# Kernel optimization log

Hardware: AMD Instinct MI355X
Metric: run time of the kernel (lower is better)

The kernel has to match this reference:

```python
import jax, jax.numpy as jnp
import numpy as np

N, C, H, W = 4, 128, 64, 64
HEADS, KS, RED = 4, 7, 18
D = C // HEADS


def _layernorm(x, w, b, eps=1e-5):
    mu = x.mean(axis=-1, keepdims=True)
    var = ((x - mu) ** 2).mean(axis=-1, keepdims=True)
    return (x - mu) * jax.lax.rsqrt(var + eps) * w + b


def _gelu(x):
    return jax.nn.gelu(x, approximate=False)


def setup_inputs() -> dict:
    key = jax.random.key(0)
    ks = jax.random.split(key, 16)
    s = 0.02
    inp = {
        'x': jax.random.normal(ks[0], (N, C, H, W), jnp.float32),
        'ln1_w': jnp.ones((C,), jnp.float32), 'ln1_b': jnp.zeros((C,), jnp.float32),
        'ln2_w': jnp.ones((C,), jnp.float32), 'ln2_b': jnp.zeros((C,), jnp.float32),
        'qkv_w': jax.random.normal(ks[1], (C, 3 * C), jnp.float32) * s,
        'qkv_b': jnp.zeros((3 * C,), jnp.float32),
        'proj_w': jax.random.normal(ks[2], (C, C), jnp.float32) * s,
        'proj_b': jnp.zeros((C,), jnp.float32),
        'rpb': jax.random.normal(ks[3], (HEADS, 2 * KS - 1, 2 * KS - 1), jnp.float32) * s,
        'conv1_w': jax.random.normal(ks[4], (C, C // 4), jnp.float32) * s,
        'conv1_b': jnp.zeros((C // 4,), jnp.float32),
        'conv2_w': jax.random.normal(ks[5], (C // 4, C), jnp.float32) * s,
        'conv2_b': jnp.zeros((C,), jnp.float32),
        'ca1_w': jax.random.normal(ks[6], (C, C // RED), jnp.float32) * s,
        'ca1_b': jnp.zeros((C // RED,), jnp.float32),
        'ca2_w': jax.random.normal(ks[7], (C // RED, C), jnp.float32) * s,
        'ca2_b': jnp.zeros((C,), jnp.float32),
        'fc1_w': jax.random.normal(ks[8], (C, 4 * C), jnp.float32) * s,
        'fc1_b': jnp.zeros((4 * C,), jnp.float32),
        'fc2_w': jax.random.normal(ks[9], (4 * C, C), jnp.float32) * s,
        'fc2_b': jnp.zeros((C,), jnp.float32),
    }
    return inp


def _na2d(xc, qkv_w, qkv_b, rpb, proj_w, proj_b):
    # xc: [N, H, W, C] -> neighborhood attention with clamped k x k windows (NATTEN semantics)
    n, h, w, c = xc.shape
    qkv = (xc @ qkv_w + qkv_b).reshape(n, h, w, 3, HEADS, D)
    q, k, v = qkv[..., 0, :, :], qkv[..., 1, :, :], qkv[..., 2, :, :]
    q = q * (D ** -0.5)
    half = KS // 2
    ni = jnp.clip(jnp.arange(h) - half, 0, h - KS)          # window start per query row
    nj = jnp.clip(jnp.arange(w) - half, 0, w - KS)
    idx_i = ni[:, None] + jnp.arange(KS)                     # [H, KS]
    idx_j = nj[:, None] + jnp.arange(KS)                     # [W, KS]
    # gather key/value windows: [N, H, KS, W, KS, heads, D]
    kw = k[:, idx_i][:, :, :, idx_j]
    vw = v[:, idx_i][:, :, :, idx_j]
    attn = jnp.einsum('nijhd,niajbhd->nijhab', q, kw)        # [N,H,W,heads,KS,KS]
    bi = idx_i - jnp.arange(h)[:, None] + (KS - 1)           # rel-pos bias row index [H,KS]
    bj = idx_j - jnp.arange(w)[:, None] + (KS - 1)           # [W,KS]
    bias = rpb[:, bi][:, :, :, bj]                           # [heads,H,KS,W,KS]
    attn = attn + bias.transpose(1, 3, 0, 2, 4)[None]        # -> [1,H,W,heads,KS,KS]
    attn = jax.nn.softmax(attn.reshape(n, h, w, HEADS, KS * KS), axis=-1)
    attn = attn.reshape(n, h, w, HEADS, KS, KS)
    out = jnp.einsum('nijhab,niajbhd->nijhd', attn, vw).reshape(n, h, w, c)
    return out @ proj_w + proj_b


def reference(x, ln1_w, ln1_b, ln2_w, ln2_b, qkv_w, qkv_b, proj_w, proj_b, rpb,
              conv1_w, conv1_b, conv2_w, conv2_b, ca1_w, ca1_b, ca2_w, ca2_b,
              fc1_w, fc1_b, fc2_w, fc2_b):
    n, c, h, w = x.shape
    xs = x.transpose(0, 2, 3, 1).reshape(n, h * w, c)        # n (h w) c
    shortcut = xs
    xn = _layernorm(xs, ln1_w, ln1_b)
    xc = xn.reshape(n, h, w, c)
    # conv branch: 1x1 -> GELU -> 1x1 -> channel attention
    t = _gelu(xc @ conv1_w + conv1_b) @ conv2_w + conv2_b
    g = t.mean(axis=(1, 2))                                  # global avg pool [N,C]
    g = jax.nn.sigmoid(jax.nn.relu(g @ ca1_w + ca1_b) @ ca2_w + ca2_b)
    ca_x = (t * g[:, None, None, :]).reshape(n, h * w, c)
    # neighborhood attention branch
    na_x = _na2d(xc, qkv_w, qkv_b, rpb, proj_w, proj_b).reshape(n, h * w, c)
    x2 = shortcut + na_x + ca_x * 0.02
    m = _gelu(_layernorm(x2, ln2_w, ln2_b) @ fc1_w + fc1_b) @ fc2_w + fc2_b
    x3 = x2 + m
    return x3.reshape(n, h, w, c).transpose(0, 3, 1, 2)
```

## Files before the change

kernel.cpp:

```cpp
#include <hip/hip_runtime.h>
#include <hip/hip_bf16.h>
#include <math.h>

#define NB 4
#define CC 128
#define HH 64
#define WW 64
#define HEADS 4
#define KS 7
#define DD 32
#define HW 4096
#define MTOT 16384

typedef unsigned short BF;
typedef short short8 __attribute__((ext_vector_type(8)));
typedef float floatx4 __attribute__((ext_vector_type(4)));

__device__ __forceinline__ float gelu_f(float x) {
    return 0.5f * x * (1.0f + erff(x * 0.70710678118654752440f));
}

__device__ __forceinline__ BF f2bf(float f) {
    union { float f; unsigned u; } a; a.f = f;
    unsigned u = a.u;
    unsigned r = u + 0x7FFFu + ((u >> 16) & 1u);
    return (BF)(r >> 16);
}

__device__ __forceinline__ float bf2f(BF v) {
    return __uint_as_float(((unsigned)v) << 16);
}

#define LDK 40
#define LDK128 136

__global__ __launch_bounds__(256) void ln1t_kernel(
    const float* __restrict__ x, const float* __restrict__ w,
    const float* __restrict__ b, BF* __restrict__ out,
    float* __restrict__ part,
    const float* __restrict__ qkv_w, const float* __restrict__ conv1_w,
    const float* __restrict__ conv2_w, const float* __restrict__ proj_w,
    const float* __restrict__ fc1_w, const float* __restrict__ fc2_w,
    BF* __restrict__ qkvT, BF* __restrict__ c1T, BF* __restrict__ c2T,
    BF* __restrict__ projT, BF* __restrict__ fc1T, BF* __restrict__ fc2T)
{
    const int blk = blockIdx.x;
    const int t  = threadIdx.x;

    if (blk >= 512) {
        for (int idx = (blk - 512) * 256 + t; idx < 204800; idx += 32768) {
            if (idx < 49152) {
                int l = idx, n = l >> 7, k = l & 127;
                qkvT[l] = f2bf(qkv_w[k * 384 + n]);
            } else if (idx < 53248) {
                int l = idx - 49152, n = l >> 7, k = l & 127;
                c1T[l] = f2bf(conv1_w[k * 32 + n]);
            } else if (idx < 57344) {
                int l = idx - 53248, n = l >> 5, k = l & 31;
                c2T[l] = f2bf(conv2_w[k * 128 + n]);
            } else if (idx < 73728) {
                int l = idx - 57344, n = l >> 7, k = l & 127;
                projT[l] = f2bf(proj_w[k * 128 + n]);
            } else if (idx < 139264) {
                int l = idx - 73728, n = l >> 7, k = l & 127;
                fc1T[l] = f2bf(fc1_w[k * 512 + n]);
            } else {
                int l = idx - 139264, n = l >> 9, k = l & 511;
                fc2T[l] = f2bf(fc2_w[k * 128 + n]);
            }
        }
        return;
    }

    __shared__ float xt[128][33];
    __shared__ float mus[32], rss[32];
    const int n  = blk >> 7;
    const int p0 = (blk & 127) * 32;
    if (blk < 4 && t < 128) part[blk * CC + t] = 0.f;

    {
        int pp = t & 31, c8 = t >> 5;
        #pragma unroll 4
        for (int it = 0; it < 16; it++) {
            int c = it * 8 + c8;
            xt[c][pp] = x[(size_t)(n * CC + c) * HW + p0 + pp];
        }
    }
    __syncthreads();
    {
        int pp2 = t >> 3, cb = t & 7;
        float s = 0.f;
        #pragma unroll
        for (int u = 0; u < 16; u++) s += xt[cb + u * 8][pp2];
        s += __shfl_xor(s, 1); s += __shfl_xor(s, 2); s += __shfl_xor(s, 4);
        float mu = s * (1.0f / CC);
        float v = 0.f;
        #pragma unroll
        for (int u = 0; u < 16; u++) { float d = xt[cb + u * 8][pp2] - mu; v += d * d; }
        v += __shfl_xor(v, 1); v += __shfl_xor(v, 2); v += __shfl_xor(v, 4);
        if (cb == 0) { mus[pp2] = mu; rss[pp2] = rsqrtf(v * (1.0f / CC) + 1e-5f); }
    }
    __syncthreads();
    {
        #pragma unroll
        for (int it = 0; it < 2; it++) {
            int pp2 = (t >> 4) + it * 16;
            int c0  = (t & 15) * 8;
            float mu = mus[pp2], rs = rss[pp2];
            int m = n * HW + p0 + pp2;
            short8 o;
            #pragma unroll
            for (int u = 0; u < 8; u++)
                o[u] = (short)f2bf((xt[c0 + u][pp2] - mu) * rs * w[c0 + u] + b[c0 + u]);
            *(short8*)(out + (size_t)m * CC + c0) = o;
        }
    }
}

template<int ACT>
__device__ __forceinline__ void k128_body(
    const BF* __restrict__ A, const BF* __restrict__ Bt,
    const float* __restrict__ bias, BF* __restrict__ Cout,
    int N, int row0, int col0, BF* Bl )
{
    const int t = threadIdx.x;
    const int w = t >> 6, lane = t & 63, q = lane >> 4, r16 = lane & 15;
    {
        int nn = t >> 2;
        int kk = (t & 3) * 32;
        const BF* src = Bt + (size_t)(col0 + nn) * 128 + kk;
        #pragma unroll
        for (int u = 0; u < 4; u++)
            *(uint4*)(Bl + nn * LDK128 + kk + u * 8) = *(const uint4*)(src + u * 8);
    }
    __syncthreads();
    floatx4 acc[4] = {};
    const BF* arow = A + (size_t)(row0 + w * 16 + r16) * CC;
    #pragma unroll
    for (int ks = 0; ks < 4; ks++) {
        short8 af = *(const short8*)(arow + ks * 32 + q * 8);
        #pragma unroll
        for (int nt = 0; nt < 4; nt++) {
            short8 bf = *(const short8*)(Bl + (nt * 16 + r16) * LDK128 + ks * 32 + q * 8);
            acc[nt] = __builtin_amdgcn_mfma_f32_16x16x32_bf16(af, bf, acc[nt], 0, 0, 0);
        }
    }
    #pragma unroll
    for (int nt = 0; nt < 4; nt++) {
        int col = col0 + nt * 16 + r16;
        float bv = bias[col];
        #pragma unroll
        for (int reg = 0; reg < 4; reg++) {
            int row = row0 + w * 16 + q * 4 + reg;
            float v = acc[nt][reg] + bv;
            if (ACT == 1) v = gelu_f(v);
            Cout[(size_t)row * N + col] = f2bf(v);
        }
    }
}

__global__ __launch_bounds__(256) void phase2(
    const BF* __restrict__ xn, const BF* __restrict__ qkvT,
    const float* __restrict__ qkv_b, BF* __restrict__ qkv_out,
    const BF* __restrict__ c1T, const float* __restrict__ b1,
    const BF* __restrict__ c2T, const float* __restrict__ b2,
    BF* __restrict__ tout, float* __restrict__ part)
{
    __shared__ __align__(16) char smem[26624];
    const int bid = blockIdx.x;
    const int t = threadIdx.x;
    const int w = t >> 6, lane = t & 63, q = lane >> 4, r16 = lane & 15;

    if (bid < 1536) {
        int col0 = (bid % 6) * 64;
        int row0 = (bid / 6) * 64;
        k128_body<0>(xn, qkvT, qkv_b, qkv_out, 384, row0, col0, (BF*)smem);
        return;
    }
    BF*    W1l = (BF*)smem;
    BF*    W2l = (BF*)(smem + 8704);
    BF*    Hl  = (BF*)(smem + 18944);
    float* red = (float*)(smem + 24064);
    const int row0 = (bid - 1536) * 64;
    {
        #pragma unroll
        for (int it = 0; it < 2; it++) {
            int idx = it * 256 + t;
            int nn = idx >> 4, u = idx & 15;
            *(uint4*)(W1l + nn * LDK128 + u * 8) = *(const uint4*)(c1T + nn * 128 + u * 8);
        }
    }
    {
        #pragma unroll
        for (int it = 0; it < 2; it++) {
            int idx = it * 256 + t;
            int nn = idx >> 2, u = idx & 3;
            *(uint4*)(W2l + nn * LDK + u * 8) = *(const uint4*)(c2T + nn * 32 + u * 8);
        }
    }
    __syncthreads();
    floatx4 a1[2] = {};
    const BF* arow = xn + (size_t)(row0 + w * 16 + r16) * CC;
    #pragma unroll
    for (int ks = 0; ks < 4; ks++) {
        short8 af = *(const short8*)(arow + ks * 32 + q * 8);
        #pragma unroll
        for (int nt = 0; nt < 2; nt++) {
            short8 bf = *(const short8*)(W1l + (nt * 16 + r16) * LDK128 + ks * 32 + q * 8);
            a1[nt] = __builtin_amdgcn_mfma_f32_16x16x32_bf16(af, bf, a1[nt], 0, 0, 0);
        }
    }
    #pragma unroll
    for (int nt = 0; nt < 2; nt++) {
        int col = nt * 16 + r16;
        float bv = b1[col];
        #pragma unroll
        for (int reg = 0; reg < 4; reg++)
            Hl[(w * 16 + q * 4 + reg) * LDK + col] = f2bf(gelu_f(a1[nt][reg] + bv));
    }
    __syncthreads();
    floatx4 a2[8] = {};
    short8 af2 = *(const short8*)(Hl + (w * 16 + r16) * LDK + q * 8);
    #pragma unroll
    for (int nt = 0; nt < 8; nt++) {
        short8 bf = *(const short8*)(W2l + (nt * 16 + r16) * LDK + q * 8);
        a2[nt] = __builtin_amdgcn_mfma_f32_16x16x32_bf16(af2, bf, a2[nt], 0, 0, 0);
    }
    #pragma unroll
    for (int nt = 0; nt < 8; nt++) {
        int col = nt * 16 + r16;
        float bv = b2[col];
        float s = 0.f;
        #pragma unroll
        for (int reg = 0; reg < 4; reg++) {
            int row = row0 + w * 16 + q * 4 + reg;
            float v = a2[nt][reg] + bv;
            tout[(size_t)row * CC + col] = f2bf(v);
            s += v;
        }
        s += __shfl_xor(s, 16);
        s += __shfl_xor(s, 32);
        if (lane < 16) red[w * 128 + col] = s;
    }
    __syncthreads();
    if (t < 128) {
        float cs = red[t] + red[128 + t] + red[256 + t] + red[384 + t];
        atomicAdd(&part[(row0 >> 12) * CC + t], cs);
    }
}

template<int ACT>
__global__ __launch_bounds__(256) void gemm_k128(
    const BF* __restrict__ A, const BF* __restrict__ Bt,
    const float* __restrict__ bias, BF* __restrict__ Cout, int N)
{
    __shared__ __align__(16) BF Bl[64 * LDK128];
    k128_body<ACT>(A, Bt, bias, Cout, N, blockIdx.y * 64, blockIdx.x * 64, Bl);
}

__global__ __launch_bounds__(256) void na_mfma_kernel(
    const BF* __restrict__ qkv, const float* __restrict__ rpb,
    BF* __restrict__ outp)
{
    __shared__ __align__(16) BF Kt[224][40];
    __shared__ __align__(16) BF Vt[32][232];
    __shared__ __align__(16) BF Qb[64][40];
    __shared__ __align__(16) BF Pl[4][16][232];
    __shared__ float rb[169];

    const int b = blockIdx.x;
    const int h = b & 3;
    const int tile = b >> 2;
    const int n = tile >> 6;
    const int ti = (tile >> 3) & 7, tj = tile & 7;
    const int t = threadIdx.x;
    const int w = t >> 6, lane = t & 63, quad = lane >> 4, r16 = lane & 15;
    const int i0 = ti * 8, j0 = tj * 8;
    const int wi0 = max(i0 - 3, 0), wj0 = max(j0 - 3, 0);
    const int R  = min(wi0 + 13, 63) - wi0 + 1;
    const int Rj = min(wj0 + 13, 63) - wj0 + 1;

    for (int idx = t; idx < 896; idx += 256) {
        int key = idx >> 2, ch = idx & 3;
        int kr = key >> 4, kc = key & 15;
        uint4 v = {0u, 0u, 0u, 0u};
        if (kr < R && kc < Rj) {
            size_t pix = (size_t)((n * HH + wi0 + kr) * WW + wj0 + kc);
            v = *(const uint4*)(qkv + pix * 384 + 128 + h * DD + ch * 8);
        }
        *(uint4*)&Kt[key][ch * 8] = v;
    }
    for (int idx = t; idx < 896; idx += 256) {
        int key = idx >> 2, ch = idx & 3;
        int kr = key >> 4, kc = key & 15;
        if (kr < R && kc < Rj) {
            size_t pix = (size_t)((n * HH + wi0 + kr) * WW + wj0 + kc);
            uint4 v = *(const uint4*)(qkv + pix * 384 + 256 + h * DD + ch * 8);
            const BF* pv = (const BF*)&v;
            #pragma unroll
            for (int u = 0; u < 8; u++) Vt[ch * 8 + u][key] = pv[u];
        } else {
            #pragma unroll
            for (int u = 0; u < 8; u++) Vt[ch * 8 + u][key] = 0;
        }
    }
    {
        int q = t >> 2, ch = t & 3;
        size_t mq = (size_t)((n * HH + i0 + (q >> 3)) * WW + j0 + (q & 7));
        *(uint4*)&Qb[q][ch * 8] = *(const uint4*)(qkv + mq * 384 + h * DD + ch * 8);
    }
    if (t < 169) rb[t] = rpb[h * 169 + t];
    __syncthreads();

    int oi[4], cok[4], bj0[4], ai_[4];
    #pragma unroll
    for (int reg = 0; reg < 4; reg++) {
        int q = w * 16 + quad * 4 + reg;
        int i = i0 + (q >> 3), j = j0 + (q & 7);
        int ni = min(max(i - 3, 0), HH - KS), nj = min(max(j - 3, 0), WW - KS);
        oi[reg]  = ni - wi0;
        ai_[reg] = ni - i + 6;
        int dc = r16 - (nj - wj0);
        cok[reg] = ((unsigned)dc < 7u) ? 1 : 0;
        bj0[reg] = min(max(dc + (nj - j + 6), 0), 12);
    }

    short8 aq = *(const short8*)&Qb[w * 16 + r16][quad * 8];
    floatx4 S[14];
    #pragma unroll
    for (int nt = 0; nt < 14; nt++) {
        floatx4 z = {0.f, 0.f, 0.f, 0.f};
        short8 bk = *(const short8*)&Kt[nt * 16 + r16][quad * 8];
        S[nt] = __builtin_amdgcn_mfma_f32_16x16x32_bf16(aq, bk, z, 0, 0, 0);
    }
    const float scale = 0.17677669529663688110f;
    #pragma unroll
    for (int nt = 0; nt < 14; nt++) {
        #pragma unroll
        for (int reg = 0; reg < 4; reg++) {
            int dr = nt - oi[reg];
            bool ok = ((unsigned)dr < 7u) && cok[reg];
            int bi = min(max(dr + ai_[reg], 0), 12);
            float bias = rb[bi * 13 + bj0[reg]];
            S[nt][reg] = ok ? fmaf(S[nt][reg], scale, bias) : -1e30f;
        }
    }
    float rinv[4];
    #pragma unroll
    for (int reg = 0; reg < 4; reg++) {
        float m = S[0][reg];
        #pragma unroll
        for (int nt = 1; nt < 14; nt++) m = fmaxf(m, S[nt][reg]);
        m = fmaxf(m, __shfl_xor(m, 1));
        m = fmaxf(m, __shfl_xor(m, 2));
        m = fmaxf(m, __shfl_xor(m, 4));
        m = fmaxf(m, __shfl_xor(m, 8));
        float s = 0.f;
        #pragma unroll
        for (int nt = 0; nt < 14; nt++) {
            float e = __expf(S[nt][reg] - m);
            S[nt][reg] = e;
            s += e;
        }
        s += __shfl_xor(s, 1);
        s += __shfl_xor(s, 2);
        s += __shfl_xor(s, 4);
        s += __shfl_xor(s, 8);
        rinv[reg] = 1.0f / s;
    }
    #pragma unroll
    for (int nt = 0; nt < 14; nt++)
        #pragma unroll
        for (int reg = 0; reg < 4; reg++)
            Pl[w][quad * 4 + reg][nt * 16 + r16] = f2bf(S[nt][reg] * rinv[reg]);

    floatx4 O0 = {0.f, 0.f, 0.f, 0.f}, O1 = {0.f, 0.f, 0.f, 0.f};
    #pragma unroll
    for (int ks = 0; ks < 7; ks++) {
        short8 ap = *(const short8*)&Pl[w][r16][ks * 32 + quad * 8];
        short8 b0 = *(const short8*)&Vt[r16][ks * 32 + quad * 8];
        short8 b1 = *(const short8*)&Vt[16 + r16][ks * 32 + quad * 8];
        O0 = __builtin_amdgcn_mfma_f32_16x16x32_bf16(ap, b0, O0, 0, 0, 0);
        O1 = __builtin_amdgcn_mfma_f32_16x16x32_bf16(ap, b1, O1, 0, 0, 0);
    }
    #pragma unroll
    for (int reg = 0; reg < 4; reg++) {
        int q = w * 16 + quad * 4 + reg;
        size_t m = (size_t)((n * HH + i0 + (q >> 3)) * WW + j0 + (q & 7));
        outp[m * CC + h * DD + r16]      = f2bf(O0[reg]);
        outp[m * CC + h * DD + 16 + r16] = f2bf(O1[reg]);
    }
}

__global__ __launch_bounds__(256) void projx2ln2g(
    const BF* __restrict__ A, const BF* __restrict__ projT,
    const float* __restrict__ bias, const float* __restrict__ x,
    const BF* __restrict__ tbuf, const float* __restrict__ part,
    const float* __restrict__ ca1_w, const float* __restrict__ ca1_b,
    const float* __restrict__ ca2_w, const float* __restrict__ ca2_b,
    const float* __restrict__ w2, const float* __restrict__ b2,
    float* __restrict__ x2b, BF* __restrict__ lnout)
{
    __shared__ __align__(16) BF Bl[128 * LDK128];
    __shared__ float xs[64][132];
    __shared__ float gs[128];
    __shared__ float h1[7];
    __shared__ float gl[128];

    const int t = threadIdx.x;
    const int w = t >> 6, lane = t & 63, q = lane >> 4, r16 = lane & 15;
    const int row0 = blockIdx.x * 64;
    const int n = row0 >> 12;
    const int p0 = row0 & 4095;

    {
        #pragma unroll
        for (int it = 0; it < 8; it++) {
            int idx = it * 256 + t;
            int nn = idx >> 4, u = idx & 15;
            *(uint4*)(Bl + nn * LDK128 + u * 8) = *(const uint4*)(projT + nn * 128 + u * 8);
        }
    }
    {
        #pragma unroll
        for (int it = 0; it < 8; it++) {
            int idx4 = it * 256 + t;
            int p4 = idx4 & 15, c = idx4 >> 4;
            float4 v = *(const float4*)(x + (size_t)(n * CC + c) * HW + p0 + p4 * 4);
            xs[p4 * 4 + 0][c] = v.x; xs[p4 * 4 + 1][c] = v.y;
            xs[p4 * 4 + 2][c] = v.z; xs[p4 * 4 + 3][c] = v.w;
        }
    }
    if (t < 128) gs[t] = part[n * CC + t] * (1.0f / HW);
    __syncthreads();
    if (t < 7) {
        float a = ca1_b[t];
        for (int k = 0; k < 128; k++) a += gs[k] * ca1_w[k * 7 + t];
        h1[t] = fmaxf(a, 0.f);
    }
    __syncthreads();
    if (t < 128) {
        float o = ca2_b[t];
        #pragma unroll
        for (int r = 0; r < 7; r++) o += h1[r] * ca2_w[r * 128 + t];
        gl[t] = 1.0f / (1.0f + expf(-o));
    }

    floatx4 acc[8] = {};
    const BF* arow = A + (size_t)(row0 + w * 16 + r16) * CC;
    #pragma unroll
    for (int ks = 0; ks < 4; ks++) {
        short8 af = *(const short8*)(arow + ks * 32 + q * 8);
        #pragma unroll
        for (int nt = 0; nt < 8; nt++) {
            short8 bf = *(const short8*)(Bl + (nt * 16 + r16) * LDK128 + ks * 32 + q * 8);
            acc[nt] = __builtin_amdgcn_mfma_f32_16x16x32_bf16(af, bf, acc[nt], 0, 0, 0);
        }
    }
    __syncthreads();

    float s1[4] = {0.f, 0.f, 0.f, 0.f}, s2[4] = {0.f, 0.f, 0.f, 0.f};
    #pragma unroll
    for (int nt = 0; nt < 8; nt++) {
        int col = nt * 16 + r16;
        float bv = bias[col];
        float gv = gl[col];
        #pragma unroll
        for (int reg = 0; reg < 4; reg++) {
            int lr = w * 16 + q * 4 + reg;
            int row = row0 + lr;
            float xv = xs[lr][col];
            float tv = bf2f(tbuf[(size_t)row * CC + col]);
            float v = acc[nt][reg] + bv + xv + 0.02f * tv * gv;
            acc[nt][reg] = v;
            s1[reg] += v;
            s2[reg] += v * v;
        }
    }
    #pragma unroll
    for (int reg = 0; reg < 4; reg++) {
        #pragma unroll
        for (int off = 8; off; off >>= 1) {
            s1[reg] += __shfl_xor(s1[reg], off);
            s2[reg] += __shfl_xor(s2[reg], off);
        }
    }
    float mu[4], rr[4];
    #pragma unroll
    for (int reg = 0; reg < 4; reg++) {
        mu[reg] = s1[reg] * (1.0f / CC);
        float var = s2[reg] * (1.0f / CC) - mu[reg] * mu[reg];
        rr[reg] = rsqrtf(var + 1e-5f);
    }
    #pragma unroll
    for (int nt = 0; nt < 8; nt++) {
        int col = nt * 16 + r16;
        float wv = w2[col], bv2 = b2[col];
        #pragma unroll
        for (int reg = 0; reg < 4; reg++) {
            int row = row0 + w * 16 + q * 4 + reg;
            float v = acc[nt][reg];
            x2b[(size_t)row * CC + col] = v;
            lnout[(size_t)row * CC + col] = f2bf((v - mu[reg]) * rr[reg] * wv + bv2);
        }
    }
}

__global__ __launch_bounds__(256) void fc2_kernel(
    const BF* __restrict__ A, const BF* __restrict__ fc2T,
    const float* __restrict__ bias, const float* __restrict__ x2b,
    float* __restrict__ out)
{
    __shared__ __align__(16) BF Alds[64][LDK];
    __shared__ __align__(16) BF Blds[64][LDK];
    __shared__ float st[64][66];

    const int t    = threadIdx.x;
    const int w    = t >> 6;
    const int lane = t & 63;
    const int q    = lane >> 4;
    const int r16  = lane & 15;
    const int row0 = blockIdx.y * 64;
    const int col0 = blockIdx.x * 64;
    const int n    = row0 >> 12;
    const int p0   = row0 & 4095;

    floatx4 acc[4] = {};
    const int ar = t >> 2;
    const int ak = (t & 3) * 8;
    const int bnn = t >> 2;
    const int bko = (t & 3) * 8;

    for (int k0 = 0; k0 < 512; k0 += 32) {
        *(short8*)(&Alds[ar][ak]) =
            *(const short8*)(A + (size_t)(row0 + ar) * 512 + k0 + ak);
        *(uint4*)(&Blds[bnn][bko]) =
            *(const uint4*)(fc2T + (size_t)(col0 + bnn) * 512 + k0 + bko);
        __syncthreads();
        short8 af = *(const short8*)(&Alds[w * 16 + r16][q * 8]);
        short8 bfm[4];
        #pragma unroll
        for (int nt = 0; nt < 4; nt++)
            bfm[nt] = *(const short8*)(&Blds[nt * 16 + r16][q * 8]);
        #pragma unroll
        for (int nt = 0; nt < 4; nt++)
            acc[nt] = __builtin_amdgcn_mfma_f32_16x16x32_bf16(af, bfm[nt], acc[nt], 0, 0, 0);
        __syncthreads();
    }

    #pragma unroll
    for (int nt = 0; nt < 4; nt++) {
        int col = col0 + nt * 16 + r16;
        float bv = bias[col];
        #pragma unroll
        for (int reg = 0; reg < 4; reg++) {
            int lr = w * 16 + q * 4 + reg;
            int row = row0 + lr;
            st[nt * 16 + r16][lr] = acc[nt][reg] + bv + x2b[(size_t)row * CC + col];
        }
    }
    __syncthreads();
    {
        int cc = t >> 2, ch = (t & 3) * 16;
        float* dst = out + (size_t)(n * CC + col0 + cc) * HW + p0 + ch;
        #pragma unroll
        for (int u = 0; u < 4; u++) {
            float4 v;
            v.x = st[cc][ch + u * 4 + 0];
            v.y = st[cc][ch + u * 4 + 1];
            v.z = st[cc][ch + u * 4 + 2];
            v.w = st[cc][ch + u * 4 + 3];
            *(float4*)(dst + u * 4) = v;
        }
    }
}

extern "C" void kernel_launch(void* const* d_in, const int* in_sizes, int n_in,
                              void* d_out, int out_size, void* d_ws, size_t ws_size,
                              hipStream_t stream)
{
    const float* x       = (const float*)d_in[0];
    const float* ln1_w   = (const float*)d_in[1];
    const float* ln1_b   = (const float*)d_in[2];
    const float* ln2_w   = (const float*)d_in[3];
    const float* ln2_b   = (const float*)d_in[4];
    const float* qkv_w   = (const float*)d_in[5];
    const float* qkv_b   = (const float*)d_in[6];
    const float* proj_w  = (const float*)d_in[7];
    const float* proj_b  = (const float*)d_in[8];
    const float* rpb     = (const float*)d_in[9];
    const float* conv1_w = (const float*)d_in[10];
    const float* conv1_b = (const float*)d_in[11];
    const float* conv2_w = (const float*)d_in[12];
    const float* conv2_b = (const float*)d_in[13];
    const float* ca1_w   = (const float*)d_in[14];
    const float* ca1_b   = (const float*)d_in[15];
    const float* ca2_w   = (const float*)d_in[16];
    const float* ca2_b   = (const float*)d_in[17];
    const float* fc1_w   = (const float*)d_in[18];
    const float* fc1_b   = (const float*)d_in[19];
    const float* fc2_w   = (const float*)d_in[20];
    const float* fc2_b   = (const float*)d_in[21];
    float* out = (float*)d_out;

    char* ws = (char*)d_ws;
    BF*    xn_bf   = (BF*)(ws);
    BF*    qkv_bf  = (BF*)(ws + 4194304);
    BF*    hbuf_bf = (BF*)(ws);
    BF*    t_bf    = (BF*)(ws + 16777216);
    float* x2b     = (float*)(ws + 25165824);
    BF*    na_bf   = (BF*)(ws + 33554432);
    BF*    ln2_bf  = (BF*)(ws + 37748736);
    float* part    = (float*)(ws + 41943040);
    BF*    qkvT    = (BF*)(ws + 41945088);
    BF*    c1T     = (BF*)(ws + 42043392);
    BF*    c2T     = (BF*)(ws + 42051584);
    BF*    projT   = (BF*)(ws + 42059776);
    BF*    fc1T    = (BF*)(ws + 42092544);
    BF*    fc2T    = (BF*)(ws + 42223616);

    ln1t_kernel<<<640, 256, 0, stream>>>(x, ln1_w, ln1_b, xn_bf, part,
        qkv_w, conv1_w, conv2_w, proj_w, fc1_w, fc2_w,
        qkvT, c1T, c2T, projT, fc1T, fc2T);
    phase2<<<1792, 256, 0, stream>>>(xn_bf, qkvT, qkv_b, qkv_bf,
                                     c1T, conv1_b, c2T, conv2_b, t_bf, part);
    na_mfma_kernel<<<1024, 256, 0, stream>>>(qkv_bf, rpb, na_bf);
    projx2ln2g<<<256, 256, 0, stream>>>(na_bf, projT, proj_b, x, t_bf, part,
                                        ca1_w, ca1_b, ca2_w, ca2_b,
                                        ln2_w, ln2_b, x2b, ln2_bf);
    gemm_k128<1><<<dim3(8, 256), 256, 0, stream>>>(ln2_bf, fc1T, fc1_b, hbuf_bf, 512);
    fc2_kernel<<<dim3(2, 256), 256, 0, stream>>>(hbuf_bf, fc2T, fc2_b, x2b, out);
}
```

Measured before the change: 174.6 us.

## Fuse proj, LN2, fc1+GELU, fc2 into one tail kernel per 32 rows

Merges the proj+residual+LN2 kernel, the fc1 GEMM and the fc2 GEMM into one kernel. Each block handles 32 rows and keeps x2, the LN2 output and the 512-wide hidden activations in LDS and registers. This removes the global round trips for x2b, ln2_bf and the large hidden buffer, plus two launches. Weights are repacked into a k-slab-major layout so the MFMA B fragments load straight from global/L2 instead of going through LDS. The trade-offs are heavy LDS use (about 60KB per block), which limits occupancy, and only 512 blocks, each re-reading all of the weights.

```diff
diff --git a/kernel.cpp b/kernel.cpp
--- a/kernel.cpp
+++ b/kernel.cpp
@@ -42,7 +42,7 @@
     const float* __restrict__ conv2_w, const float* __restrict__ proj_w,
     const float* __restrict__ fc1_w, const float* __restrict__ fc2_w,
     BF* __restrict__ qkvT, BF* __restrict__ c1T, BF* __restrict__ c2T,
-    BF* __restrict__ projT, BF* __restrict__ fc1T, BF* __restrict__ fc2T)
+    BF* __restrict__ projT2, BF* __restrict__ fc1T2, BF* __restrict__ fc2T2)
 {
     const int blk = blockIdx.x;
     const int t  = threadIdx.x;
@@ -59,14 +59,14 @@
                 int l = idx - 53248, n = l >> 5, k = l & 31;
                 c2T[l] = f2bf(conv2_w[k * 128 + n]);
             } else if (idx < 73728) {
-                int l = idx - 57344, n = l >> 7, k = l & 127;
-                projT[l] = f2bf(proj_w[k * 128 + n]);
+                int l = idx - 57344, kk = l & 31, n = (l >> 5) & 127, ks = l >> 12;
+                projT2[l] = f2bf(proj_w[(ks * 32 + kk) * 128 + n]);
             } else if (idx < 139264) {
-                int l = idx - 73728, n = l >> 7, k = l & 127;
-                fc1T[l] = f2bf(fc1_w[k * 512 + n]);
+                int l = idx - 73728, kk = l & 31, n = (l >> 5) & 511, ks = l >> 14;
+                fc1T2[l] = f2bf(fc1_w[(ks * 32 + kk) * 512 + n]);
             } else {
-                int l = idx - 139264, n = l >> 9, k = l & 511;
-                fc2T[l] = f2bf(fc2_w[k * 128 + n]);
+                int l = idx - 139264, kk = l & 31, n = (l >> 5) & 127, ks = l >> 12;
+                fc2T2[l] = f2bf(fc2_w[(ks * 32 + kk) * 128 + n]);
             }
         }
         return;
@@ -247,15 +247,6 @@
         float cs = red[t] + red[128 + t] + red[256 + t] + red[384 + t];
         atomicAdd(&part[(row0 >> 12) * CC + t], cs);
     }
-}
-
-template<int ACT>
-__global__ __launch_bounds__(256) void gemm_k128(
-    const BF* __restrict__ A, const BF* __restrict__ Bt,
-    const float* __restrict__ bias, BF* __restrict__ Cout, int N)
-{
-    __shared__ __align__(16) BF Bl[64 * LDK128];
-    k128_body<ACT>(A, Bt, bias, Cout, N, blockIdx.y * 64, blockIdx.x * 64, Bl);
 }
 
 __global__ __launch_bounds__(256) void na_mfma_kernel(
@@ -392,89 +383,81 @@
     }
 }
 
-__global__ __launch_bounds__(256) void projx2ln2g(
-    const BF* __restrict__ A, const BF* __restrict__ projT,
-    const float* __restrict__ bias, const float* __restrict__ x,
+__global__ __launch_bounds__(256) void tail_kernel(
+    const BF* __restrict__ A, const BF* __restrict__ projT2,
+    const float* __restrict__ proj_b, const float* __restrict__ x,
     const BF* __restrict__ tbuf, const float* __restrict__ part,
     const float* __restrict__ ca1_w, const float* __restrict__ ca1_b,
     const float* __restrict__ ca2_w, const float* __restrict__ ca2_b,
     const float* __restrict__ w2, const float* __restrict__ b2,
-    float* __restrict__ x2b, BF* __restrict__ lnout)
+    const BF* __restrict__ fc1T2, const float* __restrict__ fc1_b,
+    const BF* __restrict__ fc2T2, const float* __restrict__ fc2_b,
+    float* __restrict__ out)
 {
-    __shared__ __align__(16) BF Bl[128 * LDK128];
-    __shared__ float xs[64][132];
-    __shared__ float gs[128];
-    __shared__ float h1[7];
-    __shared__ float gl[128];
+    __shared__ float xs[32][132];
+    __shared__ __align__(16) BF ln2l[32][136];
+    __shared__ __align__(16) BF hl[32][520];
+    __shared__ float st[128][34];
+    __shared__ float gs[128], h1s[7], gl[128];
+    __shared__ float S1[4][16], S2[4][16];
 
     const int t = threadIdx.x;
-    const int w = t >> 6, lane = t & 63, q = lane >> 4, r16 = lane & 15;
-    const int row0 = blockIdx.x * 64;
-    const int n = row0 >> 12;
-    const int p0 = row0 & 4095;
-
-    {
-        #pragma unroll
-        for (int it = 0; it < 8; it++) {
-            int idx = it * 256 + t;
-            int nn = idx >> 4, u = idx & 15;
-            *(uint4*)(Bl + nn * LDK128 + u * 8) = *(const uint4*)(projT + nn * 128 + u * 8);
-        }
-    }
-    {
-        #pragma unroll
-        for (int it = 0; it < 8; it++) {
-            int idx4 = it * 256 + t;
-            int p4 = idx4 & 15, c = idx4 >> 4;
-            float4 v = *(const float4*)(x + (size_t)(n * CC + c) * HW + p0 + p4 * 4);
-            xs[p4 * 4 + 0][c] = v.x; xs[p4 * 4 + 1][c] = v.y;
-            xs[p4 * 4 + 2][c] = v.z; xs[p4 * 4 + 3][c] = v.w;
-        }
+    const int w = t >> 6, lane = t & 63, quad = lane >> 4, r16 = lane & 15;
+    const int row0 = blockIdx.x * 32;
+    const int n = row0 >> 12, p0 = row0 & 4095;
+    const int mt = w & 1, nh = w >> 1;
+    const int lr0 = mt * 16;
+
+    #pragma unroll
+    for (int it = 0; it < 4; it++) {
+        int idx4 = it * 256 + t;
+        int p4 = idx4 & 7, c = idx4 >> 3;
+        float4 v = *(const float4*)(x + (size_t)(n * CC + c) * HW + p0 + p4 * 4);
+        xs[p4 * 4 + 0][c] = v.x; xs[p4 * 4 + 1][c] = v.y;
+        xs[p4 * 4 + 2][c] = v.z; xs[p4 * 4 + 3][c] = v.w;
     }
     if (t < 128) gs[t] = part[n * CC + t] * (1.0f / HW);
     __syncthreads();
     if (t < 7) {
         float a = ca1_b[t];
         for (int k = 0; k < 128; k++) a += gs[k] * ca1_w[k * 7 + t];
-        h1[t] = fmaxf(a, 0.f);
+        h1s[t] = fmaxf(a, 0.f);
     }
     __syncthreads();
     if (t < 128) {
         float o = ca2_b[t];
         #pragma unroll
-        for (int r = 0; r < 7; r++) o += h1[r] * ca2_w[r * 128 + t];
+        for (int r = 0; r < 7; r++) o += h1s[r] * ca2_w[r * 128 + t];
         gl[t] = 1.0f / (1.0f + expf(-o));
     }
 
-    floatx4 acc[8] = {};
-    const BF* arow = A + (size_t)(row0 + w * 16 + r16) * CC;
+    floatx4 acc[4] = {};
+    const BF* arow = A + (size_t)(row0 + lr0 + r16) * CC;
     #pragma unroll
     for (int ks = 0; ks < 4; ks++) {
-        short8 af = *(const short8*)(arow + ks * 32 + q * 8);
-        #pragma unroll
-        for (int nt = 0; nt < 8; nt++) {
-            short8 bf = *(const short8*)(Bl + (nt * 16 + r16) * LDK128 + ks * 32 + q * 8);
+        short8 af = *(const short8*)(arow + ks * 32 + quad * 8);
+        #pragma unroll
+        for (int nt = 0; nt < 4; nt++) {
+            int col = nh * 64 + nt * 16 + r16;
+            short8 bf = *(const short8*)(projT2 + ((size_t)(ks * 128 + col)) * 32 + quad * 8);
             acc[nt] = __builtin_amdgcn_mfma_f32_16x16x32_bf16(af, bf, acc[nt], 0, 0, 0);
         }
     }
     __syncthreads();
 
+    float x2r[4][4];
     float s1[4] = {0.f, 0.f, 0.f, 0.f}, s2[4] = {0.f, 0.f, 0.f, 0.f};
     #pragma unroll
-    for (int nt = 0; nt < 8; nt++) {
-        int col = nt * 16 + r16;
-        float bv = bias[col];
-        float gv = gl[col];
+    for (int nt = 0; nt < 4; nt++) {
+        int col = nh * 64 + nt * 16 + r16;
+        float bv = proj_b[col], gv = gl[col];
         #pragma unroll
         for (int reg = 0; reg < 4; reg++) {
-            int lr = w * 16 + q * 4 + reg;
-            int row = row0 + lr;
-            float xv = xs[lr][col];
-            float tv = bf2f(tbuf[(size_t)row * CC + col]);
-            float v = acc[nt][reg] + bv + xv + 0.02f * tv * gv;
-            acc[nt][reg] = v;
-            s1[reg] += v;
-            s2[reg] += v * v;
+            int lr = lr0 + quad * 4 + reg;
+            float tv = bf2f(tbuf[(size_t)(row0 + lr) * CC + col]);
+            float v = acc[nt][reg] + bv + xs[lr][col] + 0.02f * tv * gv;
+            x2r[nt][reg] = v;
+            s1[reg] += v; s2[reg] += v * v;
         }
     }
     #pragma unroll
@@ -485,91 +468,98 @@
             s2[reg] += __shfl_xor(s2[reg], off);
         }
     }
+    if (r16 == 0) {
+        #pragma unroll
+        for (int reg = 0; reg < 4; reg++) {
+            S1[w][quad * 4 + reg] = s1[reg];
+            S2[w][quad * 4 + reg] = s2[reg];
+        }
+    }
+    __syncthreads();
+    const int pw = w ^ 2;
     float mu[4], rr[4];
     #pragma unroll
     for (int reg = 0; reg < 4; reg++) {
-        mu[reg] = s1[reg] * (1.0f / CC);
-        float var = s2[reg] * (1.0f / CC) - mu[reg] * mu[reg];
+        int r = quad * 4 + reg;
+        float t1 = S1[w][r] + S1[pw][r];
+        float t2 = S2[w][r] + S2[pw][r];
+        mu[reg] = t1 * (1.0f / CC);
+        float var = t2 * (1.0f / CC) - mu[reg] * mu[reg];
         rr[reg] = rsqrtf(var + 1e-5f);
     }
     #pragma unroll
-    for (int nt = 0; nt < 8; nt++) {
-        int col = nt * 16 + r16;
+    for (int nt = 0; nt < 4; nt++) {
+        int col = nh * 64 + nt * 16 + r16;
         float wv = w2[col], bv2 = b2[col];
         #pragma unroll
         for (int reg = 0; reg < 4; reg++) {
-            int row = row0 + w * 16 + q * 4 + reg;
-            float v = acc[nt][reg];
-            x2b[(size_t)row * CC + col] = v;
-            lnout[(size_t)row * CC + col] = f2bf((v - mu[reg]) * rr[reg] * wv + bv2);
-        }
-    }
-}
-
-__global__ __launch_bounds__(256) void fc2_kernel(
-    const BF* __restrict__ A, const BF* __restrict__ fc2T,
-    const float* __restrict__ bias, const float* __restrict__ x2b,
-    float* __restrict__ out)
-{
-    __shared__ __align__(16) BF Alds[64][LDK];
-    __shared__ __align__(16) BF Blds[64][LDK];
-    __shared__ float st[64][66];
-
-    const int t    = threadIdx.x;
-    const int w    = t >> 6;
-    const int lane = t & 63;
-    const int q    = lane >> 4;
-    const int r16  = lane & 15;
-    const int row0 = blockIdx.y * 64;
-    const int col0 = blockIdx.x * 64;
-    const int n    = row0 >> 12;
-    const int p0   = row0 & 4095;
-
-    floatx4 acc[4] = {};
-    const int ar = t >> 2;
-    const int ak = (t & 3) * 8;
-    const int bnn = t >> 2;
-    const int bko = (t & 3) * 8;
-
-    for (int k0 = 0; k0 < 512; k0 += 32) {
-        *(short8*)(&Alds[ar][ak]) =
-            *(const short8*)(A + (size_t)(row0 + ar) * 512 + k0 + ak);
-        *(uint4*)(&Blds[bnn][bko]) =
-            *(const uint4*)(fc2T + (size_t)(col0 + bnn) * 512 + k0 + bko);
-        __syncthreads();
-        short8 af = *(const short8*)(&Alds[w * 16 + r16][q * 8]);
-        short8 bfm[4];
-        #pragma unroll
-        for (int nt = 0; nt < 4; nt++)
-            bfm[nt] = *(const short8*)(&Blds[nt * 16 + r16][q * 8]);
-        #pragma unroll
-        for (int nt = 0; nt < 4; nt++)
-            acc[nt] = __builtin_amdgcn_mfma_f32_16x16x32_bf16(af, bfm[nt], acc[nt], 0, 0, 0);
-        __syncthreads();
-    }
-
+            int lr = lr0 + quad * 4 + reg;
+            ln2l[lr][col] = f2bf((x2r[nt][reg] - mu[reg]) * rr[reg] * wv + bv2);
+        }
+    }
+    __syncthreads();
+
+    short8 af1[4];
+    #pragma unroll
+    for (int ks = 0; ks < 4; ks++)
+        af1[ks] = *(const short8*)&ln2l[lr0 + r16][ks * 32 + quad * 8];
+    #pragma unroll
+    for (int g = 0; g < 4; g++) {
+        floatx4 a2[4] = {};
+        #pragma unroll
+        for (int ks = 0; ks < 4; ks++) {
+            #pragma unroll
+            for (int nt = 0; nt < 4; nt++) {
+                int col = nh * 256 + g * 64 + nt * 16 + r16;
+                short8 bf = *(const short8*)(fc1T2 + ((size_t)(ks * 512 + col)) * 32 + quad * 8);
+                a2[nt] = __builtin_amdgcn_mfma_f32_16x16x32_bf16(af1[ks], bf, a2[nt], 0, 0, 0);
+            }
+        }
+        #pragma unroll
+        for (int nt = 0; nt < 4; nt++) {
+            int col = nh * 256 + g * 64 + nt * 16 + r16;
+            float bv = fc1_b[col];
+            #pragma unroll
+            for (int reg = 0; reg < 4; reg++) {
+                int lr = lr0 + quad * 4 + reg;
+                hl[lr][col] = f2bf(gelu_f(a2[nt][reg] + bv));
+            }
+        }
+    }
+    __syncthreads();
+
+    floatx4 a3[4] = {};
+    #pragma unroll
+    for (int ks = 0; ks < 16; ks++) {
+        short8 af = *(const short8*)&hl[lr0 + r16][ks * 32 + quad * 8];
+        #pragma unroll
+        for (int nt = 0; nt < 4; nt++) {
+            int col = nh * 64 + nt * 16 + r16;
+            short8 bf = *(const short8*)(fc2T2 + ((size_t)(ks * 128 + col)) * 32 + quad * 8);
+            a3[nt] = __builtin_amdgcn_mfma_f32_16x16x32_bf16(af, bf, a3[nt], 0, 0, 0);
+        }
+    }
     #pragma unroll
     for (int nt = 0; nt < 4; nt++) {
-        int col = col0 + nt * 16 + r16;
-        float bv = bias[col];
+        int col = nh * 64 + nt * 16 + r16;
+        float bv = fc2_b[col];
         #pragma unroll
         for (int reg = 0; reg < 4; reg++) {
-            int lr = w * 16 + q * 4 + reg;
-            int row = row0 + lr;
-            st[nt * 16 + r16][lr] = acc[nt][reg] + bv + x2b[(size_t)row * CC + col];
-        }
-    }
-    __syncthreads();
-    {
-        int cc = t >> 2, ch = (t & 3) * 16;
-        float* dst = out + (size_t)(n * CC + col0 + cc) * HW + p0 + ch;
+            int lr = lr0 + quad * 4 + reg;
+            st[col][lr] = a3[nt][reg] + bv + x2r[nt][reg];
+        }
+    }
+    __syncthreads();
+    {
+        int col = t >> 1, ch = (t & 1) * 16;
+        float* dst = out + (size_t)(n * CC + col) * HW + p0 + ch;
         #pragma unroll
         for (int u = 0; u < 4; u++) {
             float4 v;
-            v.x = st[cc][ch + u * 4 + 0];
-            v.y = st[cc][ch + u * 4 + 1];
-            v.z = st[cc][ch + u * 4 + 2];
-            v.w = st[cc][ch + u * 4 + 3];
+            v.x = st[col][ch + u * 4 + 0];
+            v.y = st[col][ch + u * 4 + 1];
+            v.z = st[col][ch + u * 4 + 2];
+            v.w = st[col][ch + u * 4 + 3];
             *(float4*)(dst + u * 4) = v;
         }
     }
@@ -606,28 +596,24 @@
     char* ws = (char*)d_ws;
     BF*    xn_bf   = (BF*)(ws);
     BF*    qkv_bf  = (BF*)(ws + 4194304);
-    BF*    hbuf_bf = (BF*)(ws);
     BF*    t_bf    = (BF*)(ws + 16777216);
-    float* x2b     = (float*)(ws + 25165824);
-    BF*    na_bf   = (BF*)(ws + 33554432);
-    BF*    ln2_bf  = (BF*)(ws + 37748736);
-    float* part    = (float*)(ws + 41943040);
-    BF*    qkvT    = (BF*)(ws + 41945088);
-    BF*    c1T     = (BF*)(ws + 42043392);
-    BF*    c2T     = (BF*)(ws + 42051584);
-    BF*    projT   = (BF*)(ws + 42059776);
-    BF*    fc1T    = (BF*)(ws + 42092544);
-    BF*    fc2T    = (BF*)(ws + 42223616);
+    BF*    na_bf   = (BF*)(ws + 20971520);
+    float* part    = (float*)(ws + 25165824);
+    BF*    qkvT    = (BF*)(ws + 25167872);
+    BF*    c1T     = (BF*)(ws + 25266176);
+    BF*    c2T     = (BF*)(ws + 25274368);
+    BF*    projT2  = (BF*)(ws + 25282560);
+    BF*    fc1T2   = (BF*)(ws + 25315328);
+    BF*    fc2T2   = (BF*)(ws + 25446400);
 
     ln1t_kernel<<<640, 256, 0, stream>>>(x, ln1_w, ln1_b, xn_bf, part,
         qkv_w, conv1_w, conv2_w, proj_w, fc1_w, fc2_w,
-        qkvT, c1T, c2T, projT, fc1T, fc2T);
+        qkvT, c1T, c2T, projT2, fc1T2, fc2T2);
     phase2<<<1792, 256, 0, stream>>>(xn_bf, qkvT, qkv_b, qkv_bf,
                                      c1T, conv1_b, c2T, conv2_b, t_bf, part);
     na_mfma_kernel<<<1024, 256, 0, stream>>>(qkv_bf, rpb, na_bf);
-    projx2ln2g<<<256, 256, 0, stream>>>(na_bf, projT, proj_b, x, t_bf, part,
-                                        ca1_w, ca1_b, ca2_w, ca2_b,
-                                        ln2_w, ln2_b, x2b, ln2_bf);
-    gemm_k128<1><<<dim3(8, 256), 256, 0, stream>>>(ln2_bf, fc1T, fc1_b, hbuf_bf, 512);
-    fc2_kernel<<<dim3(2, 256), 256, 0, stream>>>(hbuf_bf, fc2T, fc2_b, x2b, out);
-}
+    tail_kernel<<<512, 256, 0, stream>>>(na_bf, projT2, proj_b, x, t_bf, part,
+                                         ca1_w, ca1_b, ca2_w, ca2_b,
+                                         ln2_w, ln2_b, fc1T2, fc1_b,
+                                         fc2T2, fc2_b, out);
+}
```

Result: no change. 172.6 us (-1.1%).
